# Performance work log

Hardware: AMD Instinct MI355X
Metric: run time of the kernel (lower is better)

## Reference

```python
import jax, jax.numpy as jnp
import numpy as np
from jax import lax

H = 8          # num_heads
LAM = 4.0      # lambda_scale
POOL = 8       # pool_ratio (effective, N % POOL == 0)
NS_ITERS = 5
NS_EPS = 1e-4
WHITE_EPS = 1e-5


def _lap_kernel(x, y):
    # x: [B,H,n,D], y: [B,H,m,D] -> exp(-||x_i - y_j||_1 / LAM): [B,H,n,m]
    l1 = jnp.sum(jnp.abs(x[:, :, :, None, :] - y[:, :, None, :, :]), axis=-1)
    return jnp.exp(-l1 / LAM)


def setup_inputs() -> dict:
    key = jax.random.key(0)
    ks = jax.random.split(key, 8)
    B, N, C = 2, 1024, 512
    s = 0.05  # weight scale for realistic magnitudes
    return {
        "x": jax.random.normal(ks[0], (B, N, C), jnp.float32),
        "attention_mask": jnp.ones((B, N), jnp.float32),
        "qkv_w": jax.random.normal(ks[1], (3 * C, C), jnp.float32) * s,
        "qkv_b": jax.random.normal(ks[2], (3 * C,), jnp.float32) * s,
        "proj_w": jax.random.normal(ks[3], (C, C), jnp.float32) * s,
        "proj_b": jax.random.normal(ks[4], (C,), jnp.float32) * s,
        "dwc_w": jax.random.normal(ks[5], (C, 1, 3), jnp.float32) * s,
        "dwc_b": jax.random.normal(ks[6], (C,), jnp.float32) * s,
    }


def reference(x, attention_mask, qkv_w, qkv_b, proj_w, proj_b, dwc_w, dwc_b):
    B, N, C = x.shape
    D = C // H
    tm = attention_mask                      # [B,N]
    mh = tm[:, None, :, None]                # [B,1,N,1] broadcast over heads

    qkv = (x @ qkv_w.T + qkv_b).reshape(B, N, 3, H, D).transpose(2, 0, 3, 1, 4)
    q, k, v = qkv[0] * mh, qkv[1] * mh, qkv[2] * mh   # [B,H,N,D]

    # NOTE: faithful to source: raw reshape of [B,N,H*D] into [B,C,N]
    v_sp = v.transpose(0, 2, 1, 3).reshape(B, C, N)
    q_sp = q.transpose(0, 2, 1, 3).reshape(B, C, N)
    k_sp = k.transpose(0, 2, 1, 3).reshape(B, C, N)

    # depthwise conv1d, kernel 3, padding 1
    v_local = lax.conv_general_dilated(
        v_sp, dwc_w, window_strides=(1,), padding=[(1, 1)],
        feature_group_count=C, dimension_numbers=("NCH", "OIH", "NCH")
    ) + dwc_b[None, :, None]
    v_local = v_local.transpose(0, 2, 1) * tm[:, :, None]   # [B,N,C]

    p = POOL
    m = N // p
    pm = tm.reshape(B, 1, m, p).mean(-1)                    # [B,1,m]
    pms = jnp.clip(pm, 1e-6)
    q_pool = (q_sp * tm[:, None, :]).reshape(B, C, m, p).mean(-1) / pms
    k_pool = (k_sp * tm[:, None, :]).reshape(B, C, m, p).mean(-1) / pms
    lmask = (pm > 0).astype(x.dtype)[:, 0, :]               # [B,m]

    q_l = q_pool.transpose(0, 2, 1).reshape(B, m, H, D).transpose(0, 2, 1, 3)
    k_l = k_pool.transpose(0, 2, 1).reshape(B, m, H, D).transpose(0, 2, 1, 3)

    W = _lap_kernel(q_l, k_l)                               # [B,H,m,m]
    pair = lmask[:, None, :, None] * lmask[:, None, None, :]
    I = jnp.eye(m, dtype=x.dtype)[None, None]
    W = W * pair + I * (1.0 - pair)

    # Newton-Schulz pseudo-inverse
    W_eps = W + NS_EPS * I
    fro = jnp.sqrt(jnp.sum(W_eps * W_eps, axis=(-2, -1), keepdims=True))
    X = (2.0 / (fro + 1e-8)) * jnp.swapaxes(W_eps, -2, -1)
    for _ in range(NS_ITERS):
        X = X @ (2.0 * I - W_eps @ X)
    W_inv = X

    la_mask = lmask[:, None, None, :]                        # [B,1,1,m]
    C_q = _lap_kernel(q, k_l) * la_mask                      # [B,H,N,m]
    C_k = _lap_kernel(k, q_l) * la_mask                      # [B,H,N,m]

    # batch-statistics whitening of C_q over dims (0,2)
    qmask = tm[:, None, :, None]                             # [B,1,N,1]
    valid = jnp.clip(jnp.sum(qmask, axis=(0, 2), keepdims=True), 1.0)
    mu = jnp.sum(C_q * qmask, axis=(0, 2), keepdims=True) / valid
    cen = (C_q - mu) * qmask
    var = jnp.sum(cen * cen, axis=(0, 2), keepdims=True) / valid
    C_q_norm = ((C_q - mu) / jnp.sqrt(var + WHITE_EPS)) * qmask

    context = W_inv @ (jnp.swapaxes(C_k, -2, -1) @ v)        # [B,H,m,D]
    ga = (C_q_norm @ context) * mh                           # [B,H,N,D]
    ga = ga.transpose(0, 2, 1, 3).reshape(B, N, C)

    out = (ga + v_local) @ proj_w.T + proj_b
    return out * tm[:, :, None]
```

## Files before the change

kernel.cpp:

```cpp
#include <hip/hip_runtime.h>
#include <hip/hip_bf16.h>
#include <hip/hip_fp16.h>

#define Hh 8
#define Bz 2
#define Nn 1024
#define Cc 512
#define Dd 64
#define Mm 128
#define NS_EPS 1e-4f
#define WHITE_EPS 1e-5f

__device__ __forceinline__ float h2f(__half v) { return __half2float(v); }
__device__ __forceinline__ __half f2h(float v) { return __float2half(v); }

typedef _Float16 half8 __attribute__((ext_vector_type(8)));
typedef float float4v __attribute__((ext_vector_type(4)));

__global__ __launch_bounds__(256) void qkv_gemm(
    const float* __restrict__ x, const float* __restrict__ w,
    const float* __restrict__ bias, const float* __restrict__ tm,
    __half* __restrict__ Q, __half* __restrict__ K, __half* __restrict__ V) {
  __shared__ _Float16 As[128 * 40];
  __shared__ _Float16 Bs[128 * 40];
  int m0 = blockIdx.x * 128, n0 = blockIdx.y * 128;
  int tid = threadIdx.x;
  int lane = tid & 63, wv = tid >> 6;
  int wm = (wv >> 1) * 64, wn = (wv & 1) * 64;
  int l15 = lane & 15, quad = lane >> 4;
  int srow = tid >> 1, shalf = tid & 1;
  float4v acc[4][4] = {};
  for (int k0 = 0; k0 < 512; k0 += 32) {
    __syncthreads();
    {
      const float4* ga = (const float4*)(x + (size_t)(m0 + srow) * 512 + k0 + shalf * 16);
      const float4* gb = (const float4*)(w + (size_t)(n0 + srow) * 512 + k0 + shalf * 16);
      float4 a0 = ga[0], a1 = ga[1], a2 = ga[2], a3 = ga[3];
      float4 b0 = gb[0], b1 = gb[1], b2 = gb[2], b3 = gb[3];
      half8 ha0 = {(_Float16)a0.x, (_Float16)a0.y, (_Float16)a0.z, (_Float16)a0.w,
                   (_Float16)a1.x, (_Float16)a1.y, (_Float16)a1.z, (_Float16)a1.w};
      half8 ha1 = {(_Float16)a2.x, (_Float16)a2.y, (_Float16)a2.z, (_Float16)a2.w,
                   (_Float16)a3.x, (_Float16)a3.y, (_Float16)a3.z, (_Float16)a3.w};
      half8 hb0 = {(_Float16)b0.x, (_Float16)b0.y, (_Float16)b0.z, (_Float16)b0.w,
                   (_Float16)b1.x, (_Float16)b1.y, (_Float16)b1.z, (_Float16)b1.w};
      half8 hb1 = {(_Float16)b2.x, (_Float16)b2.y, (_Float16)b2.z, (_Float16)b2.w,
                   (_Float16)b3.x, (_Float16)b3.y, (_Float16)b3.z, (_Float16)b3.w};
      int lo = srow * 40 + shalf * 16;
      *(half8*)&As[lo] = ha0;
      *(half8*)&As[lo + 8] = ha1;
      *(half8*)&Bs[lo] = hb0;
      *(half8*)&Bs[lo + 8] = hb1;
    }
    __syncthreads();
    half8 a[4], b[4];
#pragma unroll
    for (int mt = 0; mt < 4; ++mt)
      a[mt] = *(const half8*)&As[(wm + mt * 16 + l15) * 40 + quad * 8];
#pragma unroll
    for (int nt = 0; nt < 4; ++nt)
      b[nt] = *(const half8*)&Bs[(wn + nt * 16 + l15) * 40 + quad * 8];
#pragma unroll
    for (int mt = 0; mt < 4; ++mt)
#pragma unroll
      for (int nt = 0; nt < 4; ++nt)
        acc[mt][nt] =
            __builtin_amdgcn_mfma_f32_16x16x32_f16(a[mt], b[nt], acc[mt][nt], 0, 0, 0);
  }
#pragma unroll
  for (int mt = 0; mt < 4; ++mt) {
#pragma unroll
    for (int r = 0; r < 4; ++r) {
      int row = m0 + wm + mt * 16 + quad * 4 + r;
      int b_ = row >> 10, n_ = row & 1023;
      float t = tm[b_ * 1024 + n_];
#pragma unroll
      for (int nt = 0; nt < 4; ++nt) {
        int c3 = n0 + wn + nt * 16 + l15;
        float v = (acc[mt][nt][r] + bias[c3]) * t;
        int sec = c3 >> 9, ch = c3 & 511;
        __half* dst = (sec == 0) ? Q : (sec == 1 ? K : V);
        dst[(size_t)b_ * (Nn * Cc) + (size_t)n_ * 512 + ch] = f2h(v);
      }
    }
  }
}

__global__ __launch_bounds__(256) void pool_kernel(
    const __half* __restrict__ Q, const __half* __restrict__ K,
    const float* __restrict__ tm, __half* __restrict__ QL,
    __half* __restrict__ KL, float* __restrict__ LM) {
  int ut = blockIdx.x;
  int bh = blockIdx.y;
  int b = bh >> 3, h = bh & 7;
  int u0 = ut * 64;
  int delta = u0 >> 9;
  int ch0 = u0 & 511;
  __shared__ float Qs[64][65];
  __shared__ float Ks[64][65];
  int tid = threadIdx.x;
  for (int e = tid; e < 4096; e += 256) {
    int d = e >> 6, uu = e & 63;
    int row = 2 * (h * 64 + d) + delta;
    size_t gi = (size_t)b * (Nn * Cc) + (size_t)row * 512 + ch0 + uu;
    Qs[d][uu] = h2f(Q[gi]);
    Ks[d][uu] = h2f(K[gi]);
  }
  __syncthreads();
  int d = tid & 63, s = tid >> 6;
#pragma unroll
  for (int jr = 0; jr < 2; ++jr) {
    int jl = s + 4 * jr;
    int j = ut * 8 + jl;
    float pm = 0.f, sq = 0.f, sk = 0.f;
#pragma unroll
    for (int i = 0; i < 8; ++i) {
      float t = tm[b * 1024 + 8 * j + i];
      pm += t;
      sq += Qs[d][8 * jl + i] * t;
      sk += Ks[d][8 * jl + i] * t;
    }
    pm *= 0.125f;
    float pms = fmaxf(pm, 1e-6f);
    size_t oi = ((size_t)bh * 128 + j) * 64 + d;
    QL[oi] = f2h(sq * 0.125f / pms);
    KL[oi] = f2h(sk * 0.125f / pms);
    if (h == 0 && d == 0) LM[b * 128 + j] = (pm > 0.f) ? 1.f : 0.f;
  }
}

__global__ __launch_bounds__(256) void fused_phase1(
    const __half* __restrict__ Q, const __half* __restrict__ K,
    const __half* __restrict__ V, const __half* __restrict__ QL,
    const __half* __restrict__ KL, const float* __restrict__ LM,
    const float* __restrict__ tm, __half* __restrict__ Wh,
    float* __restrict__ KTVp, float* __restrict__ PS,
    __half* __restrict__ Pbuf) {
  __shared__ __align__(16) char smem[47616];
  int id = blockIdx.x;
  int tid = threadIdx.x;
  if (id < 512) {
    int jt = id & 3, bh = (id >> 2) & 15, nc = id >> 6;
    int b = bh >> 3, h = bh & 7;
    int j0 = jt * 32;
    float* kls = (float*)smem;
    float* Qs = (float*)(smem + 8704);
    float* red = (float*)(smem + 17408);
    int sr = tid >> 3, sd8 = (tid & 7) * 8;
    {
      half8 q = *(const half8*)(KL + (size_t)bh * 8192 + (size_t)(j0 + sr) * 64 + sd8);
      float4 f0 = {(float)q[0], (float)q[1], (float)q[2], (float)q[3]};
      float4 f1 = {(float)q[4], (float)q[5], (float)q[6], (float)q[7]};
      *(float4*)&kls[sr * 68 + sd8] = f0;
      *(float4*)&kls[sr * 68 + sd8 + 4] = f1;
    }
    int jq = tid & 15, nq = tid >> 4;
    int jA = j0 + jq * 2, jB = jA + 1;
    float lmA = LM[b * 128 + jA], lmB = LM[b * 128 + jB];
    float aA1 = 0.f, aA2 = 0.f, aA3 = 0.f, aB1 = 0.f, aB2 = 0.f, aB3 = 0.f;
    for (int nt = 0; nt < 4; ++nt) {
      int n0 = nc * 128 + nt * 32;
      __syncthreads();
      {
        size_t gi = (size_t)b * (Nn * Cc) + (size_t)(n0 + sr) * 512 + h * 64 + sd8;
        half8 kv = *(const half8*)(Q + gi);
        float4 k0 = {(float)kv[0], (float)kv[1], (float)kv[2], (float)kv[3]};
        float4 k1 = {(float)kv[4], (float)kv[5], (float)kv[6], (float)kv[7]};
        *(float4*)&Qs[sr * 68 + sd8] = k0;
        *(float4*)&Qs[sr * 68 + sd8 + 4] = k1;
      }
      __syncthreads();
      const float4* q0p = (const float4*)&kls[(jq * 2) * 68];
      const float4* q1p = (const float4*)&kls[(jq * 2 + 1) * 68];
      const float4* k0p = (const float4*)&Qs[(nq * 2) * 68];
      const float4* k1p = (const float4*)&Qs[(nq * 2 + 1) * 68];
      float s00 = 0.f, s01 = 0.f, s10 = 0.f, s11 = 0.f;
#pragma unroll
      for (int i = 0; i < 16; ++i) {
        int dq = (i + tid) & 15;
        float4 q0 = q0p[dq], q1 = q1p[dq];
        float4 k0 = k0p[dq], k1 = k1p[dq];
        s00 += fabsf(q0.x - k0.x) + fabsf(q0.y - k0.y) + fabsf(q0.z - k0.z) + fabsf(q0.w - k0.w);
        s01 += fabsf(q0.x - k1.x) + fabsf(q0.y - k1.y) + fabsf(q0.z - k1.z) + fabsf(q0.w - k1.w);
        s10 += fabsf(q1.x - k0.x) + fabsf(q1.y - k0.y) + fabsf(q1.z - k0.z) + fabsf(q1.w - k0.w);
        s11 += fabsf(q1.x - k1.x) + fabsf(q1.y - k1.y) + fabsf(q1.z - k1.z) + fabsf(q1.w - k1.w);
      }
      int nA = n0 + nq * 2, nB = nA + 1;
      float tA = tm[b * 1024 + nA], tB = tm[b * 1024 + nB];
      float xAa = expf(-s00 * 0.25f) * lmA;
      float xAb = expf(-s01 * 0.25f) * lmA;
      float xBa = expf(-s10 * 0.25f) * lmB;
      float xBb = expf(-s11 * 0.25f) * lmB;
      Pbuf[((size_t)bh * 1024 + nA) * 128 + jA] = f2h(xAa);
      Pbuf[((size_t)bh * 1024 + nB) * 128 + jA] = f2h(xAb);
      Pbuf[((size_t)bh * 1024 + nA) * 128 + jB] = f2h(xBa);
      Pbuf[((size_t)bh * 1024 + nB) * 128 + jB] = f2h(xBb);
      float xt;
      xt = xAa * tA; aA1 += xt; aA2 += xt * xt; aA3 += xt * tA;
      xt = xAb * tB; aA1 += xt; aA2 += xt * xt; aA3 += xt * tB;
      xt = xBa * tA; aB1 += xt; aB2 += xt * xt; aB3 += xt * tA;
      xt = xBb * tB; aB1 += xt; aB2 += xt * xt; aB3 += xt * tB;
    }
    int jl = jq * 2;
    red[(jl * 8 + nq) * 3 + 0] = aA1;
    red[(jl * 8 + nq) * 3 + 1] = aA2;
    red[(jl * 8 + nq) * 3 + 2] = aA3;
    red[((jl + 1) * 8 + nq) * 3 + 0] = aB1;
    red[((jl + 1) * 8 + nq) * 3 + 1] = aB2;
    red[((jl + 1) * 8 + nq) * 3 + 2] = aB3;
    __syncthreads();
    if (tid < 32) {
      float s1 = 0.f, s2 = 0.f, s3 = 0.f;
#pragma unroll
      for (int q = 0; q < 8; ++q) {
        s1 += red[(tid * 8 + q) * 3 + 0];
        s2 += red[(tid * 8 + q) * 3 + 1];
        s3 += red[(tid * 8 + q) * 3 + 2];
      }
      size_t base = ((size_t)(nc * 16 + bh) * 128 + j0 + tid) * 3;
      PS[base] = s1; PS[base + 1] = s2; PS[base + 2] = s3;
    }
  } else if (id < 768) {
    int kid = id - 512;
    int jt = kid & 3, bh = (kid >> 2) & 15, nc = kid >> 6;
    int b = bh >> 3, h = bh & 7;
    int j0 = jt * 32;
    float* qls = (float*)smem;
    float* Ks = (float*)(smem + 8704);
    float* Vs = (float*)(smem + 17408);
    float* P = (float*)(smem + 26112);
    int sr = tid >> 3, sd8 = (tid & 7) * 8;
    {
      half8 q = *(const half8*)(QL + (size_t)bh * 8192 + (size_t)(j0 + sr) * 64 + sd8);
      float4 f0 = {(float)q[0], (float)q[1], (float)q[2], (float)q[3]};
      float4 f1 = {(float)q[4], (float)q[5], (float)q[6], (float)q[7]};
      *(float4*)&qls[sr * 68 + sd8] = f0;
      *(float4*)&qls[sr * 68 + sd8 + 4] = f1;
    }
    int jq = tid & 15, nq = tid >> 4;
    int dq2 = tid & 7, jl = tid >> 3;
    float acc[8] = {};
    for (int nt = 0; nt < 8; ++nt) {
      int n0 = nc * 256 + nt * 32;
      __syncthreads();
      {
        size_t gi = (size_t)b * (Nn * Cc) + (size_t)(n0 + sr) * 512 + h * 64 + sd8;
        half8 kv = *(const half8*)(K + gi);
        half8 vv = *(const half8*)(V + gi);
        float4 k0 = {(float)kv[0], (float)kv[1], (float)kv[2], (float)kv[3]};
        float4 k1 = {(float)kv[4], (float)kv[5], (float)kv[6], (float)kv[7]};
        float4 v0 = {(float)vv[0], (float)vv[1], (float)vv[2], (float)vv[3]};
        float4 v1 = {(float)vv[4], (float)vv[5], (float)vv[6], (float)vv[7]};
        *(float4*)&Ks[sr * 68 + sd8] = k0;
        *(float4*)&Ks[sr * 68 + sd8 + 4] = k1;
        *(float4*)&Vs[sr * 68 + sd8] = v0;
        *(float4*)&Vs[sr * 68 + sd8 + 4] = v1;
      }
      __syncthreads();
      {
        const float4* q0p = (const float4*)&qls[(jq * 2) * 68];
        const float4* q1p = (const float4*)&qls[(jq * 2 + 1) * 68];
        const float4* k0p = (const float4*)&Ks[(nq * 2) * 68];
        const float4* k1p = (const float4*)&Ks[(nq * 2 + 1) * 68];
        float s00 = 0.f, s01 = 0.f, s10 = 0.f, s11 = 0.f;
#pragma unroll
        for (int i = 0; i < 16; ++i) {
          int dq = (i + tid) & 15;
          float4 q0 = q0p[dq], q1 = q1p[dq];
          float4 k0 = k0p[dq], k1 = k1p[dq];
          s00 += fabsf(q0.x - k0.x) + fabsf(q0.y - k0.y) + fabsf(q0.z - k0.z) + fabsf(q0.w - k0.w);
          s01 += fabsf(q0.x - k1.x) + fabsf(q0.y - k1.y) + fabsf(q0.z - k1.z) + fabsf(q0.w - k1.w);
          s10 += fabsf(q1.x - k0.x) + fabsf(q1.y - k0.y) + fabsf(q1.z - k0.z) + fabsf(q1.w - k0.w);
          s11 += fabsf(q1.x - k1.x) + fabsf(q1.y - k1.y) + fabsf(q1.z - k1.z) + fabsf(q1.w - k1.w);
        }
        P[(nq * 2) * 36 + jq * 2] = expf(-s00 * 0.25f);
        P[(nq * 2) * 36 + jq * 2 + 1] = expf(-s10 * 0.25f);
        P[(nq * 2 + 1) * 36 + jq * 2] = expf(-s01 * 0.25f);
        P[(nq * 2 + 1) * 36 + jq * 2 + 1] = expf(-s11 * 0.25f);
      }
      __syncthreads();
      {
#pragma unroll 4
        for (int n = 0; n < 32; ++n) {
          float p = P[n * 36 + jl];
          float4 v0 = *(const float4*)&Vs[n * 68 + dq2 * 8];
          float4 v1 = *(const float4*)&Vs[n * 68 + dq2 * 8 + 4];
          acc[0] += p * v0.x; acc[1] += p * v0.y; acc[2] += p * v0.z; acc[3] += p * v0.w;
          acc[4] += p * v1.x; acc[5] += p * v1.y; acc[6] += p * v1.z; acc[7] += p * v1.w;
        }
      }
    }
    {
      float lm = LM[b * 128 + j0 + jl];
      float* dst = &KTVp[((size_t)nc * 16 + bh) * 8192 + (size_t)(j0 + jl) * 64 + dq2 * 8];
      float4 o0 = {acc[0] * lm, acc[1] * lm, acc[2] * lm, acc[3] * lm};
      float4 o1 = {acc[4] * lm, acc[5] * lm, acc[6] * lm, acc[7] * lm};
      *(float4*)dst = o0;
      *(float4*)(dst + 4) = o1;
    }
  } else {
    int wid = id - 768;
    int it = wid >> 4, bh = wid & 15;
    int b = bh >> 3;
    int i0 = it * 16;
    float* kls = (float*)smem;
    float* qs = (float*)(smem + 34816);
    float* ps = (float*)(smem + 39168);
    for (int e = tid; e < 8192; e += 256)
      kls[(e >> 6) * 68 + (e & 63)] = h2f(KL[(size_t)bh * 8192 + e]);
    for (int e = tid; e < 1024; e += 256)
      qs[(e >> 6) * 68 + (e & 63)] =
          h2f(QL[(size_t)bh * 8192 + (size_t)(i0 + (e >> 6)) * 64 + (e & 63)]);
    __syncthreads();
    int jg = tid & 63, ng = tid >> 6;
    int j = jg * 2;
    const float4* kA = (const float4*)&kls[j * 68];
    const float4* kB = (const float4*)&kls[(j + 1) * 68];
    float sA[4] = {}, sB[4] = {};
#pragma unroll
    for (int i = 0; i < 16; ++i) {
      int dq = (i + jg) & 15;
      float4 ka = kA[dq];
      float4 kb = kB[dq];
#pragma unroll
      for (int r = 0; r < 4; ++r) {
        float4 qv = *(const float4*)&qs[(ng * 4 + r) * 68 + dq * 4];
        sA[r] += fabsf(qv.x - ka.x) + fabsf(qv.y - ka.y) + fabsf(qv.z - ka.z) + fabsf(qv.w - ka.w);
        sB[r] += fabsf(qv.x - kb.x) + fabsf(qv.y - kb.y) + fabsf(qv.z - kb.z) + fabsf(qv.w - kb.w);
      }
    }
    float lmA = LM[b * Mm + j], lmB = LM[b * Mm + j + 1];
#pragma unroll
    for (int r = 0; r < 4; ++r) {
      int i = i0 + ng * 4 + r;
      float lmi = LM[b * Mm + i];
      float prA = lmi * lmA, prB = lmi * lmB;
      float dA = (i == j) ? 1.f : 0.f;
      float dB = (i == j + 1) ? 1.f : 0.f;
      ps[(ng * 4 + r) * 132 + j] = expf(-sA[r] * 0.25f) * prA + dA * (1.f - prA) + dA * NS_EPS;
      ps[(ng * 4 + r) * 132 + j + 1] = expf(-sB[r] * 0.25f) * prB + dB * (1.f - prB) + dB * NS_EPS;
    }
    __syncthreads();
    for (int e = tid; e < 2048; e += 256)
      Wh[(size_t)bh * (Mm * Mm) + (size_t)(i0 + (e >> 7)) * 128 + (e & 127)] =
          f2h(ps[(e >> 7) * 132 + (e & 127)]);
  }
}

__global__ __launch_bounds__(256) void fused_phase2(
    const __half* __restrict__ Wh, float* __restrict__ Xout,
    const float* __restrict__ PS, const float* __restrict__ tm,
    float* __restrict__ MU, float* __restrict__ RS) {
  __shared__ __align__(16) char smem[140288];
  int tid = threadIdx.x;
  if (blockIdx.x < 16) {
    int bh = blockIdx.x;
    _Float16* Ws = (_Float16*)smem;
    _Float16* Xa = (_Float16*)(smem + 34816);
    _Float16* Xb = (_Float16*)(smem + 69632);
    _Float16* Tt = (_Float16*)(smem + 104448);
    float* red = (float*)(smem + 139264);
    const __half* Wb = Wh + (size_t)bh * 16384;
    float fro = 0.f;
    for (int e = tid; e < 16384; e += 256) {
      float wv = h2f(Wb[e]);
      Ws[(e >> 7) * 136 + (e & 127)] = (_Float16)wv;
      fro += wv * wv;
    }
    red[tid] = fro;
    __syncthreads();
    for (int off = 128; off > 0; off >>= 1) {
      if (tid < off) red[tid] += red[tid + off];
      __syncthreads();
    }
    float scale = 2.f / (sqrtf(red[0]) + 1e-8f);
    for (int e = tid; e < 16384; e += 256) {
      int i = e >> 7, k = e & 127;
      Xa[i * 136 + k] = (_Float16)(scale * (float)Ws[k * 136 + i]);
      Xb[i * 136 + k] = (_Float16)(scale * (float)Ws[i * 136 + k]);
    }
    __syncthreads();
    int lane = tid & 63, wv_ = tid >> 6;
    int wm = (wv_ >> 1) * 64, wn = (wv_ & 1) * 64;
    int l15 = lane & 15, quad = lane >> 4;
    for (int it = 0; it < 5; ++it) {
      {
        float4v acc[4][4] = {};
#pragma unroll
        for (int kt = 0; kt < 4; ++kt) {
          half8 a[4], b[4];
#pragma unroll
          for (int mt = 0; mt < 4; ++mt)
            a[mt] = *(const half8*)&Ws[(wm + mt * 16 + l15) * 136 + kt * 32 + quad * 8];
#pragma unroll
          for (int nt = 0; nt < 4; ++nt)
            b[nt] = *(const half8*)&Xb[(wn + nt * 16 + l15) * 136 + kt * 32 + quad * 8];
#pragma unroll
          for (int mt = 0; mt < 4; ++mt)
#pragma unroll
            for (int nt = 0; nt < 4; ++nt)
              acc[mt][nt] =
                  __builtin_amdgcn_mfma_f32_16x16x32_f16(a[mt], b[nt], acc[mt][nt], 0, 0, 0);
        }
#pragma unroll
        for (int mt = 0; mt < 4; ++mt)
#pragma unroll
          for (int r = 0; r < 4; ++r) {
            int i = wm + mt * 16 + quad * 4 + r;
#pragma unroll
            for (int nt = 0; nt < 4; ++nt) {
              int j = wn + nt * 16 + l15;
              Tt[j * 136 + i] = (_Float16)(((i == j) ? 2.f : 0.f) - acc[mt][nt][r]);
            }
          }
      }
      __syncthreads();
      {
        float4v acc[4][4] = {};
#pragma unroll
        for (int kt = 0; kt < 4; ++kt) {
          half8 a[4], b[4];
#pragma unroll
          for (int mt = 0; mt < 4; ++mt)
            a[mt] = *(const half8*)&Xa[(wm + mt * 16 + l15) * 136 + kt * 32 + quad * 8];
#pragma unroll
          for (int nt = 0; nt < 4; ++nt)
            b[nt] = *(const half8*)&Tt[(wn + nt * 16 + l15) * 136 + kt * 32 + quad * 8];
#pragma unroll
          for (int mt = 0; mt < 4; ++mt)
#pragma unroll
            for (int nt = 0; nt < 4; ++nt)
              acc[mt][nt] =
                  __builtin_amdgcn_mfma_f32_16x16x32_f16(a[mt], b[nt], acc[mt][nt], 0, 0, 0);
        }
        __syncthreads();
#pragma unroll
        for (int mt = 0; mt < 4; ++mt)
#pragma unroll
          for (int r = 0; r < 4; ++r) {
            int i = wm + mt * 16 + quad * 4 + r;
#pragma unroll
            for (int nt = 0; nt < 4; ++nt) {
              int j = wn + nt * 16 + l15;
              _Float16 v = (_Float16)acc[mt][nt][r];
              Xa[i * 136 + j] = v;
              Xb[j * 136 + i] = v;
            }
          }
      }
      __syncthreads();
    }
    for (int e = tid; e < 16384; e += 256)
      Xout[(size_t)bh * 16384 + e] = (float)Xa[(e >> 7) * 136 + (e & 127)];
  } else {
    float (*red2)[2] = (float(*)[2])smem;
    float* ts = (float*)(smem + 2048);
    float a = 0.f, c = 0.f;
    for (int i = tid; i < 2048; i += 256) { float t = tm[i]; a += t; c += t * t; }
    red2[tid][0] = a; red2[tid][1] = c;
    __syncthreads();
    for (int off = 128; off > 0; off >>= 1) {
      if (tid < off) { red2[tid][0] += red2[tid + off][0]; red2[tid][1] += red2[tid + off][1]; }
      __syncthreads();
    }
    if (tid == 0) { ts[0] = red2[0][0]; ts[1] = red2[0][1]; }
    __syncthreads();
    int hj = (blockIdx.x - 16) * 256 + tid;
    int h = hj >> 7, j = hj & 127;
    float s1 = 0.f, s2 = 0.f, s3 = 0.f;
#pragma unroll
    for (int nc = 0; nc < 8; ++nc)
#pragma unroll
      for (int b = 0; b < 2; ++b) {
        const float* p = PS + ((size_t)(nc * 16 + b * 8 + h) * 128 + j) * 3;
        s1 += p[0]; s2 += p[1]; s3 += p[2];
      }
    float valid = fmaxf(ts[0], 1.f);
    float mu = s1 / valid;
    float var = (s2 - 2.f * mu * s3 + mu * mu * ts[1]) / valid;
    var = fmaxf(var, 0.f);
    MU[hj] = mu;
    RS[hj] = rsqrtf(var + WHITE_EPS);
  }
}

__global__ __launch_bounds__(256) void ctx_kernel(const float* __restrict__ X,
                                                  const float* __restrict__ KTVp,
                                                  __half* __restrict__ CTX) {
  int it = blockIdx.x;
  int bh = blockIdx.y;
  int i0 = it * 16;
  __shared__ __align__(16) float KTVs[8192];
  __shared__ float Xs[16][132];
  int tid = threadIdx.x;
  const float4* src = (const float4*)KTVp;
  for (int e = tid; e < 2048; e += 256) {
    float4 s = src[(size_t)bh * 2048 + e];
#pragma unroll
    for (int nc = 1; nc < 4; ++nc) {
      float4 v = src[((size_t)nc * 16 + bh) * 2048 + e];
      s.x += v.x; s.y += v.y; s.z += v.z; s.w += v.w;
    }
    *(float4*)&KTVs[e * 4] = s;
  }
  for (int e = tid; e < 2048; e += 256)
    Xs[e >> 7][e & 127] = X[(size_t)bh * 16384 + (size_t)(i0 + (e >> 7)) * 128 + (e & 127)];
  __syncthreads();
  int il = tid >> 4, dg = tid & 15;
  float a0 = 0.f, a1 = 0.f, a2 = 0.f, a3 = 0.f;
#pragma unroll 4
  for (int j = 0; j < 128; ++j) {
    float xv = Xs[il][j];
    float4 kv = *(const float4*)&KTVs[j * 64 + dg * 4];
    a0 += xv * kv.x; a1 += xv * kv.y; a2 += xv * kv.z; a3 += xv * kv.w;
  }
  size_t ob = (size_t)bh * 8192 + (size_t)(i0 + il) * 64 + dg * 4;
  CTX[ob] = f2h(a0);
  CTX[ob + 1] = f2h(a1);
  CTX[ob + 2] = f2h(a2);
  CTX[ob + 3] = f2h(a3);
}

__global__ __launch_bounds__(256) void ga_fused(
    const __half* __restrict__ Pbuf, const float* __restrict__ MU,
    const float* __restrict__ RS, const __half* __restrict__ CTXg,
    const __half* __restrict__ V, const float* __restrict__ dwc_w,
    const float* __restrict__ dwc_b, const float* __restrict__ tm,
    __half* __restrict__ VL) {
  int bh = blockIdx.y;
  int b = bh >> 3, h = bh & 7;
  int n0 = blockIdx.x * 16;
  __shared__ __half Ps[16][130];
  __shared__ __align__(16) __half2 ctx2[128][32];
  __shared__ float musr[128][2];
  int tid = threadIdx.x;
  for (int e = tid; e < 2048; e += 256)
    Ps[e >> 7][e & 127] = Pbuf[((size_t)bh * 1024 + n0 + (e >> 7)) * 128 + (e & 127)];
  {
    const __half2* cg = (const __half2*)(CTXg + (size_t)bh * 8192);
    for (int e = tid; e < 4096; e += 256) ctx2[e >> 5][e & 31] = cg[e];
  }
  if (tid < 128) { musr[tid][0] = MU[h * 128 + tid]; musr[tid][1] = RS[h * 128 + tid]; }
  __syncthreads();
  int nn = tid >> 4, dq = tid & 15;
  float a0 = 0.f, a1 = 0.f, a2 = 0.f, a3 = 0.f;
#pragma unroll 4
  for (int j = 0; j < 128; ++j) {
    float pj = (h2f(Ps[nn][j]) - musr[j][0]) * musr[j][1];
    uint2 cc = *(const uint2*)&ctx2[j][dq * 2];
    __half2 c01 = __builtin_bit_cast(__half2, cc.x);
    __half2 c23 = __builtin_bit_cast(__half2, cc.y);
    a0 += pj * h2f(c01.x); a1 += pj * h2f(c01.y);
    a2 += pj * h2f(c23.x); a3 += pj * h2f(c23.y);
  }
  int t = n0 + nn;
  float tmv = tm[b * 1024 + t];
  float t2 = tmv * tmv;
  float acc[4] = {a0 * t2, a1 * t2, a2 * t2, a3 * t2};
#pragma unroll
  for (int q = 0; q < 4; ++q) {
    int c = h * 64 + dq * 4 + q;
    float vacc = dwc_b[c];
#pragma unroll
    for (int k = 0; k < 3; ++k) {
      int u = t - 1 + k;
      if (u >= 0 && u < 1024) {
        int n = 2 * c + (u >> 9), ch = u & 511;
        vacc += dwc_w[c * 3 + k] * h2f(V[(size_t)b * (Nn * Cc) + (size_t)n * 512 + ch]);
      }
    }
    acc[q] += vacc * tmv;
  }
  size_t base = (size_t)b * (Nn * Cc) + (size_t)t * 512 + h * 64 + dq * 4;
  VL[base] = f2h(acc[0]);
  VL[base + 1] = f2h(acc[1]);
  VL[base + 2] = f2h(acc[2]);
  VL[base + 3] = f2h(acc[3]);
}

__global__ __launch_bounds__(256) void proj_gemm(
    const __half* __restrict__ Ain, const float* __restrict__ w,
    const float* __restrict__ bias, const float* __restrict__ tm,
    float* __restrict__ out) {
  __shared__ _Float16 As[128 * 40];
  __shared__ _Float16 Bs[128 * 40];
  int m0 = blockIdx.x * 128, n0 = blockIdx.y * 128;
  int tid = threadIdx.x;
  int lane = tid & 63, wv = tid >> 6;
  int wm = (wv >> 1) * 64, wn = (wv & 1) * 64;
  int l15 = lane & 15, quad = lane >> 4;
  int srow = tid >> 1, shalf = tid & 1;
  float4v acc[4][4] = {};
  for (int k0 = 0; k0 < 512; k0 += 32) {
    __syncthreads();
    {
      const half8* ga = (const half8*)(Ain + (size_t)(m0 + srow) * 512 + k0 + shalf * 16);
      const float4* gb = (const float4*)(w + (size_t)(n0 + srow) * 512 + k0 + shalf * 16);
      half8 ha0 = ga[0], ha1 = ga[1];
      float4 b0 = gb[0], b1 = gb[1], b2 = gb[2], b3 = gb[3];
      half8 hb0 = {(_Float16)b0.x, (_Float16)b0.y, (_Float16)b0.z, (_Float16)b0.w,
                   (_Float16)b1.x, (_Float16)b1.y, (_Float16)b1.z, (_Float16)b1.w};
      half8 hb1 = {(_Float16)b2.x, (_Float16)b2.y, (_Float16)b2.z, (_Float16)b2.w,
                   (_Float16)b3.x, (_Float16)b3.y, (_Float16)b3.z, (_Float16)b3.w};
      int lo = srow * 40 + shalf * 16;
      *(half8*)&As[lo] = ha0;
      *(half8*)&As[lo + 8] = ha1;
      *(half8*)&Bs[lo] = hb0;
      *(half8*)&Bs[lo + 8] = hb1;
    }
    __syncthreads();
    half8 a[4], b[4];
#pragma unroll
    for (int mt = 0; mt < 4; ++mt)
      a[mt] = *(const half8*)&As[(wm + mt * 16 + l15) * 40 + quad * 8];
#pragma unroll
    for (int nt = 0; nt < 4; ++nt)
      b[nt] = *(const half8*)&Bs[(wn + nt * 16 + l15) * 40 + quad * 8];
#pragma unroll
    for (int mt = 0; mt < 4; ++mt)
#pragma unroll
      for (int nt = 0; nt < 4; ++nt)
        acc[mt][nt] =
            __builtin_amdgcn_mfma_f32_16x16x32_f16(a[mt], b[nt], acc[mt][nt], 0, 0, 0);
  }
#pragma unroll
  for (int mt = 0; mt < 4; ++mt) {
#pragma unroll
    for (int r = 0; r < 4; ++r) {
      int row = m0 + wm + mt * 16 + quad * 4 + r;
      int b_ = row >> 10, n_ = row & 1023;
      float t = tm[b_ * 1024 + n_];
#pragma unroll
      for (int nt = 0; nt < 4; ++nt) {
        int co = n0 + wn + nt * 16 + l15;
        out[(size_t)row * 512 + co] = (acc[mt][nt][r] + bias[co]) * t;
      }
    }
  }
}

extern "C" void kernel_launch(void* const* d_in, const int* in_sizes, int n_in,
                              void* d_out, int out_size, void* d_ws, size_t ws_size,
                              hipStream_t stream) {
  const float* x      = (const float*)d_in[0];
  const float* tm     = (const float*)d_in[1];
  const float* qkv_w  = (const float*)d_in[2];
  const float* qkv_b  = (const float*)d_in[3];
  const float* proj_w = (const float*)d_in[4];
  const float* proj_b = (const float*)d_in[5];
  const float* dwc_w  = (const float*)d_in[6];
  const float* dwc_b  = (const float*)d_in[7];
  float* out = (float*)d_out;

  char* wsb = (char*)d_ws;
  __half* Qh  = (__half*)(wsb + 0);
  __half* Kh  = (__half*)(wsb + 2097152);
  float*  XA  = (float*)(wsb + 2097152);
  __half* Vh  = (__half*)(wsb + 4194304);
  __half* VLh = (__half*)(wsb + 6291456);
  float*  KTVp = (float*)(wsb + 6291456);
  __half* QLh = (__half*)(wsb + 8388608);
  __half* KLh = (__half*)(wsb + 8650752);
  float*  LM  = (float*)(wsb + 8912896);
  float*  MU  = (float*)(wsb + 8913920);
  float*  RS  = (float*)(wsb + 8918016);
  __half* CTX = (__half*)(wsb + 8922112);
  float*  PS  = (float*)(wsb + 9184256);
  __half* Wh  = (__half*)(wsb + 9380864);

  __half* Pbuf = (__half*)d_out;

  qkv_gemm<<<dim3(16, 12), 256, 0, stream>>>(x, qkv_w, qkv_b, tm, Qh, Kh, Vh);
  pool_kernel<<<dim3(16, 16), 256, 0, stream>>>(Qh, Kh, tm, QLh, KLh, LM);
  fused_phase1<<<896, 256, 0, stream>>>(Qh, Kh, Vh, QLh, KLh, LM, tm, Wh, KTVp,
                                        PS, Pbuf);
  fused_phase2<<<20, 256, 0, stream>>>(Wh, XA, PS, tm, MU, RS);
  ctx_kernel<<<dim3(8, 16), 256, 0, stream>>>(XA, KTVp, CTX);
  ga_fused<<<dim3(64, 16), 256, 0, stream>>>(Pbuf, MU, RS, CTX, Vh, dwc_w, dwc_b, tm, VLh);
  proj_gemm<<<dim3(16, 4), 256, 0, stream>>>(VLh, proj_w, proj_b, tm, out);
}
```

Before: 219.1 us.

## Fuse context matmul into Newton-Schulz kernel and widen blocks to 1024 threads

New measurement: 207.2 us. -5.4%, faster.

```diff
diff --git a/kernel.cpp b/kernel.cpp
--- a/kernel.cpp
+++ b/kernel.cpp
@@ -346,11 +346,11 @@
   }
 }
 
-__global__ __launch_bounds__(256) void fused_phase2(
-    const __half* __restrict__ Wh, float* __restrict__ Xout,
+__global__ __launch_bounds__(1024) void fused_phase2(
+    const __half* __restrict__ Wh, const float* __restrict__ KTVp,
     const float* __restrict__ PS, const float* __restrict__ tm,
-    float* __restrict__ MU, float* __restrict__ RS) {
-  __shared__ __align__(16) char smem[140288];
+    __half* __restrict__ CTX, float* __restrict__ MU, float* __restrict__ RS) {
+  __shared__ __align__(16) char smem[143360];
   int tid = threadIdx.x;
   if (blockIdx.x < 16) {
     int bh = blockIdx.x;
@@ -361,53 +361,53 @@
     float* red = (float*)(smem + 139264);
     const __half* Wb = Wh + (size_t)bh * 16384;
     float fro = 0.f;
-    for (int e = tid; e < 16384; e += 256) {
+    for (int e = tid; e < 16384; e += 1024) {
       float wv = h2f(Wb[e]);
       Ws[(e >> 7) * 136 + (e & 127)] = (_Float16)wv;
       fro += wv * wv;
     }
     red[tid] = fro;
     __syncthreads();
-    for (int off = 128; off > 0; off >>= 1) {
+    for (int off = 512; off > 0; off >>= 1) {
       if (tid < off) red[tid] += red[tid + off];
       __syncthreads();
     }
     float scale = 2.f / (sqrtf(red[0]) + 1e-8f);
-    for (int e = tid; e < 16384; e += 256) {
+    for (int e = tid; e < 16384; e += 1024) {
       int i = e >> 7, k = e & 127;
       Xa[i * 136 + k] = (_Float16)(scale * (float)Ws[k * 136 + i]);
       Xb[i * 136 + k] = (_Float16)(scale * (float)Ws[i * 136 + k]);
     }
     __syncthreads();
     int lane = tid & 63, wv_ = tid >> 6;
-    int wm = (wv_ >> 1) * 64, wn = (wv_ & 1) * 64;
+    int wm = (wv_ >> 2) * 32, wn = (wv_ & 3) * 32;
     int l15 = lane & 15, quad = lane >> 4;
     for (int it = 0; it < 5; ++it) {
       {
-        float4v acc[4][4] = {};
+        float4v acc[2][2] = {};
 #pragma unroll
         for (int kt = 0; kt < 4; ++kt) {
-          half8 a[4], b[4];
-#pragma unroll
-          for (int mt = 0; mt < 4; ++mt)
+          half8 a[2], b[2];
+#pragma unroll
+          for (int mt = 0; mt < 2; ++mt)
             a[mt] = *(const half8*)&Ws[(wm + mt * 16 + l15) * 136 + kt * 32 + quad * 8];
 #pragma unroll
-          for (int nt = 0; nt < 4; ++nt)
+          for (int nt = 0; nt < 2; ++nt)
             b[nt] = *(const half8*)&Xb[(wn + nt * 16 + l15) * 136 + kt * 32 + quad * 8];
 #pragma unroll
-          for (int mt = 0; mt < 4; ++mt)
-#pragma unroll
-            for (int nt = 0; nt < 4; ++nt)
+          for (int mt = 0; mt < 2; ++mt)
+#pragma unroll
+            for (int nt = 0; nt < 2; ++nt)
               acc[mt][nt] =
                   __builtin_amdgcn_mfma_f32_16x16x32_f16(a[mt], b[nt], acc[mt][nt], 0, 0, 0);
         }
 #pragma unroll
-        for (int mt = 0; mt < 4; ++mt)
+        for (int mt = 0; mt < 2; ++mt)
 #pragma unroll
           for (int r = 0; r < 4; ++r) {
             int i = wm + mt * 16 + quad * 4 + r;
 #pragma unroll
-            for (int nt = 0; nt < 4; ++nt) {
+            for (int nt = 0; nt < 2; ++nt) {
               int j = wn + nt * 16 + l15;
               Tt[j * 136 + i] = (_Float16)(((i == j) ? 2.f : 0.f) - acc[mt][nt][r]);
             }
@@ -415,31 +415,31 @@
       }
       __syncthreads();
       {
-        float4v acc[4][4] = {};
+        float4v acc[2][2] = {};
 #pragma unroll
         for (int kt = 0; kt < 4; ++kt) {
-          half8 a[4], b[4];
-#pragma unroll
-          for (int mt = 0; mt < 4; ++mt)
+          half8 a[2], b[2];
+#pragma unroll
+          for (int mt = 0; mt < 2; ++mt)
             a[mt] = *(const half8*)&Xa[(wm + mt * 16 + l15) * 136 + kt * 32 + quad * 8];
 #pragma unroll
-          for (int nt = 0; nt < 4; ++nt)
+          for (int nt = 0; nt < 2; ++nt)
             b[nt] = *(const half8*)&Tt[(wn + nt * 16 + l15) * 136 + kt * 32 + quad * 8];
 #pragma unroll
-          for (int mt = 0; mt < 4; ++mt)
-#pragma unroll
-            for (int nt = 0; nt < 4; ++nt)
+          for (int mt = 0; mt < 2; ++mt)
+#pragma unroll
+            for (int nt = 0; nt < 2; ++nt)
               acc[mt][nt] =
                   __builtin_amdgcn_mfma_f32_16x16x32_f16(a[mt], b[nt], acc[mt][nt], 0, 0, 0);
         }
         __syncthreads();
 #pragma unroll
-        for (int mt = 0; mt < 4; ++mt)
+        for (int mt = 0; mt < 2; ++mt)
 #pragma unroll
           for (int r = 0; r < 4; ++r) {
             int i = wm + mt * 16 + quad * 4 + r;
 #pragma unroll
-            for (int nt = 0; nt < 4; ++nt) {
+            for (int nt = 0; nt < 2; ++nt) {
               int j = wn + nt * 16 + l15;
               _Float16 v = (_Float16)acc[mt][nt][r];
               Xa[i * 136 + j] = v;
@@ -449,22 +449,42 @@
       }
       __syncthreads();
     }
-    for (int e = tid; e < 16384; e += 256)
-      Xout[(size_t)bh * 16384 + e] = (float)Xa[(e >> 7) * 136 + (e & 127)];
+    float* KTVs = (float*)smem;
+    for (int e = tid; e < 8192; e += 1024) {
+      float s = KTVp[(size_t)bh * 8192 + e];
+#pragma unroll
+      for (int nc = 1; nc < 4; ++nc) s += KTVp[((size_t)nc * 16 + bh) * 8192 + e];
+      KTVs[(e >> 6) * 68 + (e & 63)] = s;
+    }
+    __syncthreads();
+    int i = tid >> 3, d0 = (tid & 7) * 8;
+    float a0 = 0.f, a1 = 0.f, a2 = 0.f, a3 = 0.f;
+    float a4 = 0.f, a5 = 0.f, a6 = 0.f, a7 = 0.f;
+#pragma unroll 4
+    for (int j = 0; j < 128; ++j) {
+      float xv = (float)Xa[i * 136 + j];
+      float4 k0 = *(const float4*)&KTVs[j * 68 + d0];
+      float4 k1 = *(const float4*)&KTVs[j * 68 + d0 + 4];
+      a0 += xv * k0.x; a1 += xv * k0.y; a2 += xv * k0.z; a3 += xv * k0.w;
+      a4 += xv * k1.x; a5 += xv * k1.y; a6 += xv * k1.z; a7 += xv * k1.w;
+    }
+    half8 hout = {(_Float16)a0, (_Float16)a1, (_Float16)a2, (_Float16)a3,
+                  (_Float16)a4, (_Float16)a5, (_Float16)a6, (_Float16)a7};
+    *(half8*)(CTX + (size_t)bh * 8192 + (size_t)i * 64 + d0) = hout;
   } else {
     float (*red2)[2] = (float(*)[2])smem;
-    float* ts = (float*)(smem + 2048);
+    float* ts = (float*)(smem + 8192);
     float a = 0.f, c = 0.f;
-    for (int i = tid; i < 2048; i += 256) { float t = tm[i]; a += t; c += t * t; }
+    for (int i = tid; i < 2048; i += 1024) { float t = tm[i]; a += t; c += t * t; }
     red2[tid][0] = a; red2[tid][1] = c;
     __syncthreads();
-    for (int off = 128; off > 0; off >>= 1) {
+    for (int off = 512; off > 0; off >>= 1) {
       if (tid < off) { red2[tid][0] += red2[tid + off][0]; red2[tid][1] += red2[tid + off][1]; }
       __syncthreads();
     }
     if (tid == 0) { ts[0] = red2[0][0]; ts[1] = red2[0][1]; }
     __syncthreads();
-    int hj = (blockIdx.x - 16) * 256 + tid;
+    int hj = tid;
     int h = hj >> 7, j = hj & 127;
     float s1 = 0.f, s2 = 0.f, s3 = 0.f;
 #pragma unroll
@@ -481,43 +501,6 @@
     MU[hj] = mu;
     RS[hj] = rsqrtf(var + WHITE_EPS);
   }
-}
-
-__global__ __launch_bounds__(256) void ctx_kernel(const float* __restrict__ X,
-                                                  const float* __restrict__ KTVp,
-                                                  __half* __restrict__ CTX) {
-  int it = blockIdx.x;
-  int bh = blockIdx.y;
-  int i0 = it * 16;
-  __shared__ __align__(16) float KTVs[8192];
-  __shared__ float Xs[16][132];
-  int tid = threadIdx.x;
-  const float4* src = (const float4*)KTVp;
-  for (int e = tid; e < 2048; e += 256) {
-    float4 s = src[(size_t)bh * 2048 + e];
-#pragma unroll
-    for (int nc = 1; nc < 4; ++nc) {
-      float4 v = src[((size_t)nc * 16 + bh) * 2048 + e];
-      s.x += v.x; s.y += v.y; s.z += v.z; s.w += v.w;
-    }
-    *(float4*)&KTVs[e * 4] = s;
-  }
-  for (int e = tid; e < 2048; e += 256)
-    Xs[e >> 7][e & 127] = X[(size_t)bh * 16384 + (size_t)(i0 + (e >> 7)) * 128 + (e & 127)];
-  __syncthreads();
-  int il = tid >> 4, dg = tid & 15;
-  float a0 = 0.f, a1 = 0.f, a2 = 0.f, a3 = 0.f;
-#pragma unroll 4
-  for (int j = 0; j < 128; ++j) {
-    float xv = Xs[il][j];
-    float4 kv = *(const float4*)&KTVs[j * 64 + dg * 4];
-    a0 += xv * kv.x; a1 += xv * kv.y; a2 += xv * kv.z; a3 += xv * kv.w;
-  }
-  size_t ob = (size_t)bh * 8192 + (size_t)(i0 + il) * 64 + dg * 4;
-  CTX[ob] = f2h(a0);
-  CTX[ob + 1] = f2h(a1);
-  CTX[ob + 2] = f2h(a2);
-  CTX[ob + 3] = f2h(a3);
 }
 
 __global__ __launch_bounds__(256) void ga_fused(
@@ -654,7 +637,6 @@
   char* wsb = (char*)d_ws;
   __half* Qh  = (__half*)(wsb + 0);
   __half* Kh  = (__half*)(wsb + 2097152);
-  float*  XA  = (float*)(wsb + 2097152);
   __half* Vh  = (__half*)(wsb + 4194304);
   __half* VLh = (__half*)(wsb + 6291456);
   float*  KTVp = (float*)(wsb + 6291456);
@@ -673,8 +655,7 @@
   pool_kernel<<<dim3(16, 16), 256, 0, stream>>>(Qh, Kh, tm, QLh, KLh, LM);
   fused_phase1<<<896, 256, 0, stream>>>(Qh, Kh, Vh, QLh, KLh, LM, tm, Wh, KTVp,
                                         PS, Pbuf);
-  fused_phase2<<<20, 256, 0, stream>>>(Wh, XA, PS, tm, MU, RS);
-  ctx_kernel<<<dim3(8, 16), 256, 0, stream>>>(XA, KTVp, CTX);
+  fused_phase2<<<17, 1024, 0, stream>>>(Wh, KTVp, PS, tm, CTX, MU, RS);
   ga_fused<<<dim3(64, 16), 256, 0, stream>>>(Pbuf, MU, RS, CTX, Vh, dwc_w, dwc_b, tm, VLh);
   proj_gemm<<<dim3(16, 4), 256, 0, stream>>>(VLh, proj_w, proj_b, tm, out);
 }
```
